# Performance work log

Hardware: AMD Instinct MI355X
Metric: run time of the kernel (lower is better)

The kernel has to match this reference:

```python
import jax, jax.numpy as jnp
import numpy as np

K = 1024
H = 16
B = 2
T = 2048


def setup_inputs() -> dict:
    key = jax.random.key(0)
    ks = jax.random.split(key, 8)
    x = jax.random.normal(ks[0], (B, T, K), dtype=jnp.float32)
    mask = jax.random.randint(ks[1], (B, T), 0, 2, dtype=jnp.int32)
    scale = 1.0 / np.sqrt(K)
    Wk = jax.random.normal(ks[2], (K, K), dtype=jnp.float32) * scale
    Wq = jax.random.normal(ks[3], (K, K), dtype=jnp.float32) * scale
    Wv = jax.random.normal(ks[4], (K, K), dtype=jnp.float32) * scale
    Wu = jax.random.normal(ks[5], (K, K), dtype=jnp.float32) * scale
    bu = jnp.zeros((K,), dtype=jnp.float32)
    return {"x": x, "mask": mask, "Wk": Wk, "Wq": Wq, "Wv": Wv, "Wu": Wu, "bu": bu}


def reference(x, mask, Wk, Wq, Wv, Wu, bu):
    b, t, k = x.shape
    h = H
    s = k // h
    # Linear(k, k, bias=False): y = x @ W.T
    keys = (x @ Wk.T).reshape(b, t, h, s)
    queries = (x @ Wq.T).reshape(b, t, h, s)
    values = (x @ Wv.T).reshape(b, t, h, s)
    # raw scores [b, h, t, t]; NOTE: original applies NO 1/sqrt(s) scaling
    raw = jnp.einsum("bqhd,bkhd->bhqk", queries, keys)
    # mask [b, t] broadcast over heads and query positions (keys masked)
    raw = jnp.where(mask[:, None, None, :] == 0, -jnp.inf, raw)
    weights = jax.nn.softmax(raw, axis=-1)
    ys = jnp.einsum("bhqk,bkhd->bqhd", weights, values).reshape(b, t, k)
    return ys @ Wu.T + bu
```

## Files before the change

kernel.cpp:

```cpp
#include <hip/hip_runtime.h>
#include <hip/hip_bf16.h>
#include <math.h>

#define TS 2048
#define KD 1024
#define NH 16
#define SD 64
#define MB 4096
#define LOG2E 1.4426950408889634f

typedef __attribute__((ext_vector_type(8))) short bf16x8;
typedef __attribute__((ext_vector_type(4))) short bf16x4;
typedef __attribute__((ext_vector_type(4))) float f32x4;
typedef unsigned short ushort_t;

#define MFMA32(a, b, c) __builtin_amdgcn_mfma_f32_16x16x32_bf16(a, b, c, 0, 0, 0)

__device__ __forceinline__ ushort_t f2bf_rn(float f) {
    union { __hip_bfloat16 h; ushort_t u; } c;
    c.h = __float2bfloat16(f);
    return c.u;
}
__device__ __forceinline__ float bf2f(ushort_t u) {
    union { unsigned u; float f; } v; v.u = ((unsigned)u) << 16;
    return v.f;
}
__device__ __forceinline__ ushort4 pk4_bf(float a, float b, float c, float d) {
    union { __hip_bfloat162 h; ushort2 u; } x, y;
    x.h = __float22bfloat162_rn(make_float2(a, b));
    y.h = __float22bfloat162_rn(make_float2(c, d));
    return make_ushort4(x.u.x, x.u.y, y.u.x, y.u.y);
}
__device__ __forceinline__ void gload_lds16(const void* g, void* l) {
    __builtin_amdgcn_global_load_lds(
        (const __attribute__((address_space(1))) unsigned int*)g,
        (__attribute__((address_space(3))) unsigned int*)l, 16, 0, 0);
}

__global__ __launch_bounds__(256)
void conv_all(const float* __restrict__ x, const float* __restrict__ wq,
              const float* __restrict__ wk, const float* __restrict__ wv,
              const float* __restrict__ wu,
              ushort_t* XH, ushort_t* XL, ushort_t* WqH, ushort_t* WqL,
              ushort_t* WkH, ushort_t* WkL, ushort_t* WvH, ushort_t* WuH)
{
    int z = blockIdx.y;
    const float* src; ushort_t* H; ushort_t* L = nullptr; int nblk;
    switch (z) {
        case 0:  src = x;  H = XH;  L = XL;  nblk = 4096; break;
        case 1:  src = wq; H = WqH; L = WqL; nblk = 1024; break;
        case 2:  src = wk; H = WkH; L = WkL; nblk = 1024; break;
        case 3:  src = wv; H = WvH;          nblk = 1024; break;
        default: src = wu; H = WuH;          nblk = 1024; break;
    }
    if ((int)blockIdx.x >= nblk) return;
    int idx = blockIdx.x * 256 + threadIdx.x;
    float4 v = ((const float4*)src)[idx];
    if (z == 1) { v.x *= LOG2E; v.y *= LOG2E; v.z *= LOG2E; v.w *= LOG2E; }
    ushort_t h0 = f2bf_rn(v.x), h1 = f2bf_rn(v.y);
    ushort_t h2 = f2bf_rn(v.z), h3 = f2bf_rn(v.w);
    ((ushort4*)H)[idx] = make_ushort4(h0, h1, h2, h3);
    if (L) {
        ushort_t l0 = f2bf_rn(v.x - bf2f(h0)), l1 = f2bf_rn(v.y - bf2f(h1));
        ushort_t l2 = f2bf_rn(v.z - bf2f(h2)), l3 = f2bf_rn(v.w - bf2f(h3));
        ((ushort4*)L)[idx] = make_ushort4(l0, l1, l2, l3);
    }
}

__global__ __launch_bounds__(256)
void gemm_bf16(const ushort_t* __restrict__ Ah, const ushort_t* __restrict__ Al,
               const ushort_t* __restrict__ Bqh, const ushort_t* __restrict__ Bql,
               const ushort_t* __restrict__ Bkh, const ushort_t* __restrict__ Bkl,
               const ushort_t* __restrict__ Bvh, const ushort_t* __restrict__ Buh,
               ushort_t* __restrict__ OQh, ushort_t* __restrict__ OQl,
               ushort_t* __restrict__ OKh, ushort_t* __restrict__ OKl,
               ushort_t* __restrict__ OVt, float* __restrict__ OF,
               const float* __restrict__ bias, int epi_base)
{
    const int epi = epi_base + blockIdx.z;
    const ushort_t* Bh; const ushort_t* Bl = nullptr;
    if      (epi == 0) { Bh = Bqh; Bl = Bql; }
    else if (epi == 1) { Bh = Bkh; Bl = Bkl; }
    else if (epi == 2) { Bh = Bvh; }
    else               { Bh = Buh; }
    const bool terms3 = (epi < 2);

    __shared__ ushort_t sAh[128 * 32];
    __shared__ ushort_t sAl[128 * 32];
    __shared__ ushort_t sBh[128 * 32];
    __shared__ ushort_t sBl[128 * 32];

    const int tid = threadIdx.x;
    const int wave = tid >> 6, lane = tid & 63;
    const int col = lane & 15, quad = lane >> 4;
    const int wm = wave >> 1, wn = wave & 1;
    const int m0 = blockIdx.y * 128, n0 = blockIdx.x * 128;

    f32x4 acc[4][4];
#pragma unroll
    for (int i = 0; i < 4; ++i)
#pragma unroll
        for (int j = 0; j < 4; ++j) acc[i][j] = (f32x4){0.f, 0.f, 0.f, 0.f};

    for (int k0 = 0; k0 < KD; k0 += 32) {
#pragma unroll
        for (int j = 0; j < 2; ++j) {
            int s   = wave * 128 + j * 64 + lane;
            int row = s >> 2, k8 = s & 3;
            int lo  = (wave * 128 + j * 64) * 8;
            gload_lds16(Ah + (size_t)(m0 + row) * KD + k0 + k8 * 8, sAh + lo);
            gload_lds16(Bh + (size_t)(n0 + row) * KD + k0 + k8 * 8, sBh + lo);
            if (terms3) {
                gload_lds16(Al + (size_t)(m0 + row) * KD + k0 + k8 * 8, sAl + lo);
                gload_lds16(Bl + (size_t)(n0 + row) * KD + k0 + k8 * 8, sBl + lo);
            }
        }
        __syncthreads();

        bf16x8 fbh[4], fbl[4];
#pragma unroll
        for (int j = 0; j < 4; ++j) {
            int r = (wn * 64 + j * 16 + col) * 32 + quad * 8;
            fbh[j] = *(const bf16x8*)&sBh[r];
            if (terms3) fbl[j] = *(const bf16x8*)&sBl[r];
        }
#pragma unroll
        for (int i = 0; i < 4; ++i) {
            int r = (wm * 64 + i * 16 + col) * 32 + quad * 8;
            bf16x8 fah = *(const bf16x8*)&sAh[r];
            if (terms3) {
                bf16x8 fal = *(const bf16x8*)&sAl[r];
#pragma unroll
                for (int j = 0; j < 4; ++j) {
                    acc[i][j] = MFMA32(fah, fbh[j], acc[i][j]);
                    acc[i][j] = MFMA32(fah, fbl[j], acc[i][j]);
                    acc[i][j] = MFMA32(fal, fbh[j], acc[i][j]);
                }
            } else {
#pragma unroll
                for (int j = 0; j < 4; ++j)
                    acc[i][j] = MFMA32(fah, fbh[j], acc[i][j]);
            }
        }
        __syncthreads();
    }

    if (epi <= 1) {
        ushort_t* OH = (epi == 0) ? OQh : OKh;
        ushort_t* OL = (epi == 0) ? OQl : OKl;
#pragma unroll
        for (int i = 0; i < 4; ++i) {
            int m = m0 + wm * 64 + i * 16 + quad * 4;
#pragma unroll
            for (int j = 0; j < 4; ++j) {
                int n = n0 + wn * 64 + j * 16 + col;
#pragma unroll
                for (int r = 0; r < 4; ++r) {
                    float v = acc[i][j][r];
                    ushort_t hv = f2bf_rn(v);
                    size_t off = (size_t)(m + r) * KD + n;
                    OH[off] = hv;
                    OL[off] = f2bf_rn(v - bf2f(hv));
                }
            }
        }
    } else if (epi == 2) {
#pragma unroll
        for (int i = 0; i < 4; ++i) {
            int m = m0 + wm * 64 + i * 16 + quad * 4;
            int bb = m >> 11, t = m & (TS - 1);
#pragma unroll
            for (int j = 0; j < 4; ++j) {
                int n = n0 + wn * 64 + j * 16 + col;
                int hh = n >> 6, d = n & 63;
                ushort4 pk = pk4_bf(acc[i][j][0], acc[i][j][1], acc[i][j][2], acc[i][j][3]);
                *(ushort4*)(OVt + ((size_t)(bb * NH + hh) * SD + d) * TS + t) = pk;
            }
        }
    } else {
#pragma unroll
        for (int i = 0; i < 4; ++i) {
            int m = m0 + wm * 64 + i * 16 + quad * 4;
#pragma unroll
            for (int j = 0; j < 4; ++j) {
                int n = n0 + wn * 64 + j * 16 + col;
                float bj = bias[n];
#pragma unroll
                for (int r = 0; r < 4; ++r)
                    OF[(size_t)(m + r) * KD + n] = acc[i][j][r] + bj;
            }
        }
    }
}

__global__ __launch_bounds__(256, 2)
void attn_mfma(const ushort_t* __restrict__ QH, const ushort_t* __restrict__ QL,
               const ushort_t* __restrict__ KH, const ushort_t* __restrict__ KL,
               const ushort_t* __restrict__ VT, const int* __restrict__ mask,
               ushort_t* __restrict__ YH)
{
    const int qt = blockIdx.x;
    const int h  = blockIdx.y;
    const int b  = blockIdx.z;
    const int bh = b * NH + h;

    const int tid  = threadIdx.x;
    const int wave = tid >> 6;
    const int lane = tid & 63;
    const int col  = lane & 15;
    const int quad = lane >> 4;

    __shared__ ushort_t smem[24576];
    ushort_t* sKH = smem;
    ushort_t* sKL = smem + 4096;
    ushort_t* sVT = smem + 8192;
    __shared__ float lred[4][64];

    bf16x8 bqh[4][2], bql[4][2];
#pragma unroll
    for (int qf = 0; qf < 4; ++qf) {
        size_t qrow = (size_t)(b * TS + qt * 64 + qf * 16 + col) * KD + h * SD;
#pragma unroll
        for (int c = 0; c < 2; ++c) {
            bqh[qf][c] = *(const bf16x8*)(QH + qrow + c * 32 + quad * 8);
            bql[qf][c] = *(const bf16x8*)(QL + qrow + c * 32 + quad * 8);
        }
    }

    float lp[4] = {0.f, 0.f, 0.f, 0.f};
    f32x4 O[4][4];
#pragma unroll
    for (int dt = 0; dt < 4; ++dt)
#pragma unroll
        for (int qf = 0; qf < 4; ++qf) O[dt][qf] = (f32x4){0.f, 0.f, 0.f, 0.f};

    const int l8 = lane >> 3, l7 = lane & 7;

    for (int kt = 0; kt < TS / 64; ++kt) {
        const int kb = kt * 64;
#pragma unroll
        for (int r = 0; r < 6; ++r) {
            int c = r * 4 + wave;
            if (c < 8) {
                int row = c * 8 + l8;
                int gs  = l7 ^ (row & 7);
                gload_lds16(KH + (size_t)(b * TS + kb + row) * KD + h * SD + gs * 8,
                            sKH + c * 512);
            } else if (c < 16) {
                int cc = c - 8, row = cc * 8 + l8;
                int gs = l7 ^ (row & 7);
                gload_lds16(KL + (size_t)(b * TS + kb + row) * KD + h * SD + gs * 8,
                            sKL + cc * 512);
            } else {
                int cc = c - 16, row = cc * 8 + l8;
                int gs = l7 ^ (row & 7);
                gload_lds16(VT + ((size_t)bh * SD + row) * TS + kb + gs * 8,
                            sVT + cc * 512);
            }
        }
        int4 mv = *(const int4*)(mask + b * TS + kb + wave * 16 + quad * 4);
        __syncthreads();

        bf16x8 akh[2], akl[2];
#pragma unroll
        for (int c = 0; c < 2; ++c) {
            int sl = (c * 4 + quad) ^ (col & 7);
            akh[c] = *(const bf16x8*)&sKH[((wave * 16 + col) * 8 + sl) * 8];
            akl[c] = *(const bf16x8*)&sKL[((wave * 16 + col) * 8 + sl) * 8];
        }
        bf16x8 av[4];
#pragma unroll
        for (int dt = 0; dt < 4; ++dt) {
            int sl = (wave * 2 + (quad >> 1)) ^ (col & 7);
            bf16x4 v4 = *(const bf16x4*)&sVT[((dt * 16 + col) * 8 + sl) * 8 + (quad & 1) * 4];
            av[dt] = (bf16x8){v4[0], v4[1], v4[2], v4[3], 0, 0, 0, 0};
        }

        bf16x8 bp[4];
#pragma unroll
        for (int qf = 0; qf < 4; ++qf) {
            f32x4 s1 = (f32x4){0.f, 0.f, 0.f, 0.f};
            f32x4 s2 = (f32x4){0.f, 0.f, 0.f, 0.f};
            s1 = MFMA32(akh[0], bqh[qf][0], s1);
            s2 = MFMA32(akl[0], bqh[qf][0], s2);
            s2 = MFMA32(akh[0], bql[qf][0], s2);
            s1 = MFMA32(akh[1], bqh[qf][1], s1);
            s2 = MFMA32(akl[1], bqh[qf][1], s2);
            s2 = MFMA32(akh[1], bql[qf][1], s2);
            float p0 = mv.x ? exp2f(s1[0] + s2[0]) : 0.f;
            float p1 = mv.y ? exp2f(s1[1] + s2[1]) : 0.f;
            float p2 = mv.z ? exp2f(s1[2] + s2[2]) : 0.f;
            float p3 = mv.w ? exp2f(s1[3] + s2[3]) : 0.f;
            lp[qf] += (p0 + p1) + (p2 + p3);
            union { ushort4 u4; bf16x4 v4; } pk;
            pk.u4 = pk4_bf(p0, p1, p2, p3);
            bp[qf] = (bf16x8){pk.v4[0], pk.v4[1], pk.v4[2], pk.v4[3], 0, 0, 0, 0};
        }

#pragma unroll
        for (int dt = 0; dt < 4; ++dt)
#pragma unroll
            for (int qf = 0; qf < 4; ++qf)
                O[dt][qf] = MFMA32(av[dt], bp[qf], O[dt][qf]);

        __syncthreads();
    }

    float lq[4];
#pragma unroll
    for (int qf = 0; qf < 4; ++qf) {
        float v = lp[qf];
        v += __shfl_xor(v, 16);
        v += __shfl_xor(v, 32);
        lq[qf] = v;
    }
    if (lane < 16) {
#pragma unroll
        for (int qf = 0; qf < 4; ++qf) lred[wave][qf * 16 + lane] = lq[qf];
    }
    float* Ored = (float*)smem;
    if (wave > 0) {
        float* dst = Ored + (wave - 1) * 4096;
#pragma unroll
        for (int dt = 0; dt < 4; ++dt)
#pragma unroll
            for (int qf = 0; qf < 4; ++qf)
                *(f32x4*)&dst[((dt * 4 + qf) * 64 + lane) * 4] = O[dt][qf];
    }
    __syncthreads();
    if (wave == 0) {
#pragma unroll
        for (int w = 0; w < 3; ++w)
#pragma unroll
            for (int dt = 0; dt < 4; ++dt)
#pragma unroll
                for (int qf = 0; qf < 4; ++qf) {
                    f32x4 t = *(const f32x4*)&Ored[w * 4096 + ((dt * 4 + qf) * 64 + lane) * 4];
                    O[dt][qf] += t;
                }
        float linv[4];
#pragma unroll
        for (int qf = 0; qf < 4; ++qf) {
            int q = qf * 16 + col;
            linv[qf] = 1.f / (lred[0][q] + lred[1][q] + lred[2][q] + lred[3][q]);
        }
#pragma unroll
        for (int dt = 0; dt < 4; ++dt)
#pragma unroll
            for (int qf = 0; qf < 4; ++qf) {
                ushort4 pk = pk4_bf(O[dt][qf][0] * linv[qf], O[dt][qf][1] * linv[qf],
                                    O[dt][qf][2] * linv[qf], O[dt][qf][3] * linv[qf]);
                *(ushort4*)(YH + (size_t)(b * TS + qt * 64 + qf * 16 + col) * KD +
                            h * SD + dt * 16 + quad * 4) = pk;
            }
    }
}

extern "C" void kernel_launch(void* const* d_in, const int* in_sizes, int n_in,
                              void* d_out, int out_size, void* d_ws, size_t ws_size,
                              hipStream_t stream) {
    const float* x    = (const float*)d_in[0];
    const int*   mask = (const int*)d_in[1];
    const float* Wk   = (const float*)d_in[2];
    const float* Wq   = (const float*)d_in[3];
    const float* Wv   = (const float*)d_in[4];
    const float* Wu   = (const float*)d_in[5];
    const float* bu   = (const float*)d_in[6];
    float* out = (float*)d_out;

    char* w = (char*)d_ws;
    const size_t M1 = (size_t)1 << 20;
    ushort_t* XH  = (ushort_t*)(w);
    ushort_t* XL  = (ushort_t*)(w + 8  * M1);
    ushort_t* WqH = (ushort_t*)(w + 16 * M1);
    ushort_t* WqL = (ushort_t*)(w + 18 * M1);
    ushort_t* WkH = (ushort_t*)(w + 20 * M1);
    ushort_t* WkL = (ushort_t*)(w + 22 * M1);
    ushort_t* WvH = (ushort_t*)(w + 24 * M1);
    ushort_t* WuH = (ushort_t*)(w + 26 * M1);
    ushort_t* QHb = (ushort_t*)(w + 28 * M1);
    ushort_t* QLb = (ushort_t*)(w + 36 * M1);
    ushort_t* KHb = (ushort_t*)(w + 44 * M1);
    ushort_t* KLb = (ushort_t*)(w + 52 * M1);
    ushort_t* VTb = (ushort_t*)(w + 16 * M1);
    ushort_t* YHb = (ushort_t*)(w);

    dim3 blk(256);
    conv_all<<<dim3(4096, 5), blk, 0, stream>>>(x, Wq, Wk, Wv, Wu,
                                                XH, XL, WqH, WqL, WkH, WkL, WvH, WuH);
    gemm_bf16<<<dim3(8, 32, 2), blk, 0, stream>>>(XH, XL, WqH, WqL, WkH, WkL, WvH, WuH,
                                                  QHb, QLb, KHb, KLb, nullptr, nullptr,
                                                  nullptr, 0);
    gemm_bf16<<<dim3(8, 32, 1), blk, 0, stream>>>(XH, XL, WqH, WqL, WkH, WkL, WvH, WuH,
                                                  nullptr, nullptr, nullptr, nullptr, VTb,
                                                  nullptr, nullptr, 2);
    attn_mfma<<<dim3(32, NH, 2), blk, 0, stream>>>(QHb, QLb, KHb, KLb, VTb, mask, YHb);
    gemm_bf16<<<dim3(8, 32, 1), blk, 0, stream>>>(YHb, nullptr, WqH, WqL, WkH, WkL, WvH, WuH,
                                                  nullptr, nullptr, nullptr, nullptr, nullptr,
                                                  out, bu, 3);
}
```

Before: 318.1 us.

## Shrink GEMM M-tile, merge V projection launch, and streamline attention loop

The GEMM block tile drops from 128x128 to 64x128, doubling the grid and halving A-tile shared memory. The separate V-projection launch is folded into the Q/K launch via a third z-slice, and V^T is staged in the output buffer. In the attention kernel, global pointers are precomputed and incremented, the mask is applied as an initial -inf accumulator instead of per-element selects, and zero-padded fragment halves are kept persistent. The final cross-wave O reduction now runs serially through a single 16 KB buffer, halving attention shared memory at the cost of extra barriers.

```diff
diff --git a/kernel.cpp b/kernel.cpp
--- a/kernel.cpp
+++ b/kernel.cpp
@@ -15,6 +15,8 @@
 typedef unsigned short ushort_t;
 
 #define MFMA32(a, b, c) __builtin_amdgcn_mfma_f32_16x16x32_bf16(a, b, c, 0, 0, 0)
+
+union frag8 { bf16x8 v8; bf16x4 h[2]; };
 
 __device__ __forceinline__ ushort_t f2bf_rn(float f) {
     union { __hip_bfloat16 h; ushort_t u; } c;
@@ -85,8 +87,8 @@
     else               { Bh = Buh; }
     const bool terms3 = (epi < 2);
 
-    __shared__ ushort_t sAh[128 * 32];
-    __shared__ ushort_t sAl[128 * 32];
+    __shared__ ushort_t sAh[64 * 32];
+    __shared__ ushort_t sAl[64 * 32];
     __shared__ ushort_t sBh[128 * 32];
     __shared__ ushort_t sBl[128 * 32];
 
@@ -94,26 +96,30 @@
     const int wave = tid >> 6, lane = tid & 63;
     const int col = lane & 15, quad = lane >> 4;
     const int wm = wave >> 1, wn = wave & 1;
-    const int m0 = blockIdx.y * 128, n0 = blockIdx.x * 128;
-
-    f32x4 acc[4][4];
-#pragma unroll
-    for (int i = 0; i < 4; ++i)
+    const int m0 = blockIdx.y * 64, n0 = blockIdx.x * 128;
+
+    f32x4 acc[2][4];
+#pragma unroll
+    for (int i = 0; i < 2; ++i)
 #pragma unroll
         for (int j = 0; j < 4; ++j) acc[i][j] = (f32x4){0.f, 0.f, 0.f, 0.f};
 
     for (int k0 = 0; k0 < KD; k0 += 32) {
+        {
+            int row = tid >> 2, k8 = tid & 3;
+            int lo  = wave * 64 * 8;
+            gload_lds16(Ah + (size_t)(m0 + row) * KD + k0 + k8 * 8, sAh + lo);
+            if (terms3)
+                gload_lds16(Al + (size_t)(m0 + row) * KD + k0 + k8 * 8, sAl + lo);
+        }
 #pragma unroll
         for (int j = 0; j < 2; ++j) {
             int s   = wave * 128 + j * 64 + lane;
             int row = s >> 2, k8 = s & 3;
             int lo  = (wave * 128 + j * 64) * 8;
-            gload_lds16(Ah + (size_t)(m0 + row) * KD + k0 + k8 * 8, sAh + lo);
             gload_lds16(Bh + (size_t)(n0 + row) * KD + k0 + k8 * 8, sBh + lo);
-            if (terms3) {
-                gload_lds16(Al + (size_t)(m0 + row) * KD + k0 + k8 * 8, sAl + lo);
+            if (terms3)
                 gload_lds16(Bl + (size_t)(n0 + row) * KD + k0 + k8 * 8, sBl + lo);
-            }
         }
         __syncthreads();
 
@@ -125,8 +131,8 @@
             if (terms3) fbl[j] = *(const bf16x8*)&sBl[r];
         }
 #pragma unroll
-        for (int i = 0; i < 4; ++i) {
-            int r = (wm * 64 + i * 16 + col) * 32 + quad * 8;
+        for (int i = 0; i < 2; ++i) {
+            int r = (wm * 32 + i * 16 + col) * 32 + quad * 8;
             bf16x8 fah = *(const bf16x8*)&sAh[r];
             if (terms3) {
                 bf16x8 fal = *(const bf16x8*)&sAl[r];
@@ -149,8 +155,8 @@
         ushort_t* OH = (epi == 0) ? OQh : OKh;
         ushort_t* OL = (epi == 0) ? OQl : OKl;
 #pragma unroll
-        for (int i = 0; i < 4; ++i) {
-            int m = m0 + wm * 64 + i * 16 + quad * 4;
+        for (int i = 0; i < 2; ++i) {
+            int m = m0 + wm * 32 + i * 16 + quad * 4;
 #pragma unroll
             for (int j = 0; j < 4; ++j) {
                 int n = n0 + wn * 64 + j * 16 + col;
@@ -166,8 +172,8 @@
         }
     } else if (epi == 2) {
 #pragma unroll
-        for (int i = 0; i < 4; ++i) {
-            int m = m0 + wm * 64 + i * 16 + quad * 4;
+        for (int i = 0; i < 2; ++i) {
+            int m = m0 + wm * 32 + i * 16 + quad * 4;
             int bb = m >> 11, t = m & (TS - 1);
 #pragma unroll
             for (int j = 0; j < 4; ++j) {
@@ -179,8 +185,8 @@
         }
     } else {
 #pragma unroll
-        for (int i = 0; i < 4; ++i) {
-            int m = m0 + wm * 64 + i * 16 + quad * 4;
+        for (int i = 0; i < 2; ++i) {
+            int m = m0 + wm * 32 + i * 16 + quad * 4;
 #pragma unroll
             for (int j = 0; j < 4; ++j) {
                 int n = n0 + wn * 64 + j * 16 + col;
@@ -210,7 +216,7 @@
     const int col  = lane & 15;
     const int quad = lane >> 4;
 
-    __shared__ ushort_t smem[24576];
+    __shared__ ushort_t smem[12288];
     ushort_t* sKH = smem;
     ushort_t* sKL = smem + 4096;
     ushort_t* sVT = smem + 8192;
@@ -227,6 +233,21 @@
         }
     }
 
+    const int l8 = lane >> 3, l7 = lane & 7;
+    const ushort_t* gp[6];
+    ushort_t* ld[6];
+#pragma unroll
+    for (int r = 0; r < 6; ++r) {
+        int cc  = (r & 1) * 4 + wave;
+        int row = cc * 8 + l8;
+        int gs  = l7 ^ (row & 7);
+        if (r < 2)      gp[r] = KH + (size_t)(b * TS + row) * KD + h * SD + gs * 8;
+        else if (r < 4) gp[r] = KL + (size_t)(b * TS + row) * KD + h * SD + gs * 8;
+        else            gp[r] = VT + ((size_t)bh * SD + row) * TS + gs * 8;
+        ld[r] = ((r < 2) ? sKH : (r < 4) ? sKL : sVT) + cc * 512;
+    }
+    const int* mp = mask + b * TS + wave * 16 + quad * 4;
+
     float lp[4] = {0.f, 0.f, 0.f, 0.f};
     f32x4 O[4][4];
 #pragma unroll
@@ -234,32 +255,27 @@
 #pragma unroll
         for (int qf = 0; qf < 4; ++qf) O[dt][qf] = (f32x4){0.f, 0.f, 0.f, 0.f};
 
-    const int l8 = lane >> 3, l7 = lane & 7;
+    frag8 av[4], bp4[4];
+#pragma unroll
+    for (int i = 0; i < 4; ++i) {
+        av[i].v8  = (bf16x8){0, 0, 0, 0, 0, 0, 0, 0};
+        bp4[i].v8 = (bf16x8){0, 0, 0, 0, 0, 0, 0, 0};
+    }
 
     for (int kt = 0; kt < TS / 64; ++kt) {
-        const int kb = kt * 64;
-#pragma unroll
-        for (int r = 0; r < 6; ++r) {
-            int c = r * 4 + wave;
-            if (c < 8) {
-                int row = c * 8 + l8;
-                int gs  = l7 ^ (row & 7);
-                gload_lds16(KH + (size_t)(b * TS + kb + row) * KD + h * SD + gs * 8,
-                            sKH + c * 512);
-            } else if (c < 16) {
-                int cc = c - 8, row = cc * 8 + l8;
-                int gs = l7 ^ (row & 7);
-                gload_lds16(KL + (size_t)(b * TS + kb + row) * KD + h * SD + gs * 8,
-                            sKL + cc * 512);
-            } else {
-                int cc = c - 16, row = cc * 8 + l8;
-                int gs = l7 ^ (row & 7);
-                gload_lds16(VT + ((size_t)bh * SD + row) * TS + kb + gs * 8,
-                            sVT + cc * 512);
-            }
-        }
-        int4 mv = *(const int4*)(mask + b * TS + kb + wave * 16 + quad * 4);
-        __syncthreads();
+#pragma unroll
+        for (int r = 0; r < 6; ++r) gload_lds16(gp[r], ld[r]);
+        int4 mv = *(const int4*)mp;
+        mp += 64;
+#pragma unroll
+        for (int r = 0; r < 6; ++r) gp[r] += (r < 4) ? 64 * KD : 64;
+        __syncthreads();
+
+        f32x4 sinit;
+        sinit[0] = mv.x ? 0.f : -INFINITY;
+        sinit[1] = mv.y ? 0.f : -INFINITY;
+        sinit[2] = mv.z ? 0.f : -INFINITY;
+        sinit[3] = mv.w ? 0.f : -INFINITY;
 
         bf16x8 akh[2], akl[2];
 #pragma unroll
@@ -268,18 +284,15 @@
             akh[c] = *(const bf16x8*)&sKH[((wave * 16 + col) * 8 + sl) * 8];
             akl[c] = *(const bf16x8*)&sKL[((wave * 16 + col) * 8 + sl) * 8];
         }
-        bf16x8 av[4];
 #pragma unroll
         for (int dt = 0; dt < 4; ++dt) {
             int sl = (wave * 2 + (quad >> 1)) ^ (col & 7);
-            bf16x4 v4 = *(const bf16x4*)&sVT[((dt * 16 + col) * 8 + sl) * 8 + (quad & 1) * 4];
-            av[dt] = (bf16x8){v4[0], v4[1], v4[2], v4[3], 0, 0, 0, 0};
-        }
-
-        bf16x8 bp[4];
+            av[dt].h[0] = *(const bf16x4*)&sVT[((dt * 16 + col) * 8 + sl) * 8 + (quad & 1) * 4];
+        }
+
 #pragma unroll
         for (int qf = 0; qf < 4; ++qf) {
-            f32x4 s1 = (f32x4){0.f, 0.f, 0.f, 0.f};
+            f32x4 s1 = sinit;
             f32x4 s2 = (f32x4){0.f, 0.f, 0.f, 0.f};
             s1 = MFMA32(akh[0], bqh[qf][0], s1);
             s2 = MFMA32(akl[0], bqh[qf][0], s2);
@@ -287,57 +300,54 @@
             s1 = MFMA32(akh[1], bqh[qf][1], s1);
             s2 = MFMA32(akl[1], bqh[qf][1], s2);
             s2 = MFMA32(akh[1], bql[qf][1], s2);
-            float p0 = mv.x ? exp2f(s1[0] + s2[0]) : 0.f;
-            float p1 = mv.y ? exp2f(s1[1] + s2[1]) : 0.f;
-            float p2 = mv.z ? exp2f(s1[2] + s2[2]) : 0.f;
-            float p3 = mv.w ? exp2f(s1[3] + s2[3]) : 0.f;
+            float p0 = exp2f(s1[0] + s2[0]);
+            float p1 = exp2f(s1[1] + s2[1]);
+            float p2 = exp2f(s1[2] + s2[2]);
+            float p3 = exp2f(s1[3] + s2[3]);
             lp[qf] += (p0 + p1) + (p2 + p3);
             union { ushort4 u4; bf16x4 v4; } pk;
             pk.u4 = pk4_bf(p0, p1, p2, p3);
-            bp[qf] = (bf16x8){pk.v4[0], pk.v4[1], pk.v4[2], pk.v4[3], 0, 0, 0, 0};
+            bp4[qf].h[0] = pk.v4;
         }
 
 #pragma unroll
         for (int dt = 0; dt < 4; ++dt)
 #pragma unroll
             for (int qf = 0; qf < 4; ++qf)
-                O[dt][qf] = MFMA32(av[dt], bp[qf], O[dt][qf]);
-
-        __syncthreads();
-    }
-
-    float lq[4];
+                O[dt][qf] = MFMA32(av[dt].v8, bp4[qf].v8, O[dt][qf]);
+
+        __syncthreads();
+    }
+
 #pragma unroll
     for (int qf = 0; qf < 4; ++qf) {
         float v = lp[qf];
         v += __shfl_xor(v, 16);
         v += __shfl_xor(v, 32);
-        lq[qf] = v;
-    }
-    if (lane < 16) {
-#pragma unroll
-        for (int qf = 0; qf < 4; ++qf) lred[wave][qf * 16 + lane] = lq[qf];
-    }
-    float* Ored = (float*)smem;
-    if (wave > 0) {
-        float* dst = Ored + (wave - 1) * 4096;
-#pragma unroll
-        for (int dt = 0; dt < 4; ++dt)
-#pragma unroll
-            for (int qf = 0; qf < 4; ++qf)
-                *(f32x4*)&dst[((dt * 4 + qf) * 64 + lane) * 4] = O[dt][qf];
-    }
-    __syncthreads();
+        if (lane < 16) lred[wave][qf * 16 + lane] = v;
+    }
+
+    float* Of = (float*)smem;
+#pragma unroll
+    for (int w = 1; w < 4; ++w) {
+        __syncthreads();
+        if (wave == w) {
+#pragma unroll
+            for (int dt = 0; dt < 4; ++dt)
+#pragma unroll
+                for (int qf = 0; qf < 4; ++qf)
+                    *(f32x4*)&Of[((dt * 4 + qf) * 64 + lane) * 4] = O[dt][qf];
+        }
+        __syncthreads();
+        if (wave == 0) {
+#pragma unroll
+            for (int dt = 0; dt < 4; ++dt)
+#pragma unroll
+                for (int qf = 0; qf < 4; ++qf)
+                    O[dt][qf] += *(const f32x4*)&Of[((dt * 4 + qf) * 64 + lane) * 4];
+        }
+    }
     if (wave == 0) {
-#pragma unroll
-        for (int w = 0; w < 3; ++w)
-#pragma unroll
-            for (int dt = 0; dt < 4; ++dt)
-#pragma unroll
-                for (int qf = 0; qf < 4; ++qf) {
-                    f32x4 t = *(const f32x4*)&Ored[w * 4096 + ((dt * 4 + qf) * 64 + lane) * 4];
-                    O[dt][qf] += t;
-                }
         float linv[4];
 #pragma unroll
         for (int qf = 0; qf < 4; ++qf) {
@@ -377,25 +387,22 @@
     ushort_t* WkH = (ushort_t*)(w + 20 * M1);
     ushort_t* WkL = (ushort_t*)(w + 22 * M1);
     ushort_t* WvH = (ushort_t*)(w + 24 * M1);
-    ushort_t* WuH = (ushort_t*)(w + 26 * M1);
-    ushort_t* QHb = (ushort_t*)(w + 28 * M1);
-    ushort_t* QLb = (ushort_t*)(w + 36 * M1);
-    ushort_t* KHb = (ushort_t*)(w + 44 * M1);
-    ushort_t* KLb = (ushort_t*)(w + 52 * M1);
-    ushort_t* VTb = (ushort_t*)(w + 16 * M1);
+    ushort_t* QHb = (ushort_t*)(w + 26 * M1);
+    ushort_t* QLb = (ushort_t*)(w + 34 * M1);
+    ushort_t* KHb = (ushort_t*)(w + 42 * M1);
+    ushort_t* KLb = (ushort_t*)(w + 50 * M1);
+    ushort_t* WuH = (ushort_t*)(w + 58 * M1);
+    ushort_t* VTb = (ushort_t*)d_out;
     ushort_t* YHb = (ushort_t*)(w);
 
     dim3 blk(256);
     conv_all<<<dim3(4096, 5), blk, 0, stream>>>(x, Wq, Wk, Wv, Wu,
                                                 XH, XL, WqH, WqL, WkH, WkL, WvH, WuH);
-    gemm_bf16<<<dim3(8, 32, 2), blk, 0, stream>>>(XH, XL, WqH, WqL, WkH, WkL, WvH, WuH,
-                                                  QHb, QLb, KHb, KLb, nullptr, nullptr,
+    gemm_bf16<<<dim3(8, 64, 3), blk, 0, stream>>>(XH, XL, WqH, WqL, WkH, WkL, WvH, WuH,
+                                                  QHb, QLb, KHb, KLb, VTb, nullptr,
                                                   nullptr, 0);
-    gemm_bf16<<<dim3(8, 32, 1), blk, 0, stream>>>(XH, XL, WqH, WqL, WkH, WkL, WvH, WuH,
-                                                  nullptr, nullptr, nullptr, nullptr, VTb,
-                                                  nullptr, nullptr, 2);
     attn_mfma<<<dim3(32, NH, 2), blk, 0, stream>>>(QHb, QLb, KHb, KLb, VTb, mask, YHb);
-    gemm_bf16<<<dim3(8, 32, 1), blk, 0, stream>>>(YHb, nullptr, WqH, WqL, WkH, WkL, WvH, WuH,
+    gemm_bf16<<<dim3(8, 64, 1), blk, 0, stream>>>(YHb, nullptr, WqH, WqL, WkH, WkL, WvH, WuH,
                                                   nullptr, nullptr, nullptr, nullptr, nullptr,
                                                   out, bu, 3);
 }
```

New measurement: 303.6 us. 1.05x faster.
